# Kernel tuning notes

Measured on AMD Instinct MI355X. Metric: run time of the kernel, lower is better.

The kernel has to match this reference:

```python
import jax, jax.numpy as jnp
import numpy as np

N_NODES = 100000
N_EDGES = 1600000
IN_CH, HID_CH, OUT_CH = 128, 64, 32


def setup_inputs() -> dict:
    key = jax.random.key(0)
    k1, k2, k3, k4 = jax.random.split(key, 4)
    x = jax.random.normal(k1, (N_NODES, IN_CH), dtype=jnp.float32)
    edge_index = jax.random.randint(k2, (2, N_EDGES), 0, N_NODES, dtype=jnp.int32)
    # Glorot-ish scaling like PyG's GCNConv init
    W1 = jax.random.normal(k3, (IN_CH, HID_CH), dtype=jnp.float32) / np.sqrt(IN_CH)
    b1 = jnp.zeros((HID_CH,), dtype=jnp.float32)
    W2 = jax.random.normal(k4, (HID_CH, OUT_CH), dtype=jnp.float32) / np.sqrt(HID_CH)
    b2 = jnp.zeros((OUT_CH,), dtype=jnp.float32)
    return {"x": x, "edge_index": edge_index, "W1": W1, "b1": b1, "W2": W2, "b2": b2}


def reference(x, edge_index, W1, b1, W2, b2):
    # PyG GCNConv semantics: add self-loops, symmetric deg^{-1/2} normalization,
    # linear transform, scatter-add aggregation to destination nodes, add bias.
    N = x.shape[0]
    loops = jnp.arange(N, dtype=edge_index.dtype)
    src = jnp.concatenate([edge_index[0], loops])  # [E+N]
    dst = jnp.concatenate([edge_index[1], loops])  # [E+N]

    deg = jax.ops.segment_sum(jnp.ones_like(src, dtype=x.dtype), dst, num_segments=N)
    dis = jnp.where(deg > 0, jax.lax.rsqrt(jnp.maximum(deg, 1.0)), 0.0)  # deg^{-1/2}
    norm = (dis[src] * dis[dst])[:, None]  # [E+N, 1]

    def gcn_conv(h, W, b):
        h = h @ W                                   # [N, C_out]
        msgs = h[src] * norm                        # gather + scale, [E+N, C_out]
        return jax.ops.segment_sum(msgs, dst, num_segments=N) + b

    h = jax.nn.relu(gcn_conv(x, W1, b1))
    # dropout is identity in eval mode (training=False)
    return gcn_conv(h, W2, b2)
```

## Files before the change

### kernel.cpp

```cpp
#include <hip/hip_runtime.h>
#include <hip/hip_bf16.h>

#define IN_CH 128
#define HID_CH 64
#define OUT_CH 32
#define EPB 2048
#define MAXB 512

typedef unsigned short ushort_t;
typedef __attribute__((ext_vector_type(8))) short short8;
typedef __attribute__((ext_vector_type(4))) float float4v;

static __device__ __forceinline__ ushort_t f2bf(float f) {
    unsigned u = __float_as_uint(f);
    unsigned r = (u + 0x7fff + ((u >> 16) & 1)) >> 16;
    return (ushort_t)r;
}
static __device__ __forceinline__ float bf_lo(unsigned u) { return __uint_as_float(u << 16); }
static __device__ __forceinline__ float bf_hi(unsigned u) { return __uint_as_float(u & 0xffff0000u); }


__global__ __launch_bounds__(256) void k_partition(const int* __restrict__ src,
                                                   const int* __restrict__ dst,
                                                   int* __restrict__ gcursor,
                                                   unsigned* __restrict__ pairs,
                                                   int E, int nbk, int cap, int PB,
                                                   const float* __restrict__ W1,
                                                   unsigned* __restrict__ wsW) {
    __shared__ int lhist[MAXB];
    __shared__ int lbase[MAXB];
    __shared__ int lcur[MAXB];
    const int tid = threadIdx.x;

    if (blockIdx.x >= PB) {
        int s = (blockIdx.x - PB) * 256 + tid;
        int lane = s & 63;
        int nt = (s >> 6) & 3;
        int kc = s >> 8;
        int c = nt * 16 + (lane & 15);
        int k0 = kc * 32 + (lane >> 4) * 8;
        unsigned o[4];
#pragma unroll
        for (int d = 0; d < 4; ++d) {
            unsigned lo = f2bf(W1[(k0 + 2 * d) * 64 + c]);
            unsigned hi = f2bf(W1[(k0 + 2 * d + 1) * 64 + c]);
            o[d] = lo | (hi << 16);
        }
        ((uint4*)wsW)[s] = make_uint4(o[0], o[1], o[2], o[3]);
        return;
    }

    for (int b = tid; b < nbk; b += 256) { lhist[b] = 0; lcur[b] = 0; }
    __syncthreads();
    int s[8], d[8];
    const int e0 = blockIdx.x * EPB;
#pragma unroll
    for (int j = 0; j < 8; ++j) {
        int e = e0 + j * 256 + tid;
        if (e < E) {
            s[j] = src[e];
            d[j] = dst[e];
            atomicAdd(&lhist[d[j] >> 8], 1);
        } else {
            d[j] = -1;
        }
    }
    __syncthreads();
    for (int b = tid; b < nbk; b += 256)
        lbase[b] = lhist[b] ? atomicAdd(&gcursor[b], lhist[b]) : 0;
    __syncthreads();
#pragma unroll
    for (int j = 0; j < 8; ++j) {
        if (d[j] >= 0) {
            int b = d[j] >> 8;
            int loc = atomicAdd(&lcur[b], 1);
            int idx = lbase[b] + loc;
            if (idx < cap)
                pairs[(long long)b * cap + idx] = ((unsigned)s[j] << 8) | (unsigned)(d[j] & 255);
        }
    }
}


__global__ __launch_bounds__(256) void k_bucket_build(const unsigned* __restrict__ pairs,
                                                      const int* __restrict__ gcursor,
                                                      int* __restrict__ rowptr,
                                                      int* __restrict__ col,
                                                      float* __restrict__ dis,
                                                      int cap, int N) {
    __shared__ int lc[256];
    __shared__ int ls[256];
    __shared__ int lcur[256];
    const int b = blockIdx.x, tid = threadIdx.x;

    int ga = min(gcursor[2 * tid], cap);
    int gb = min(gcursor[2 * tid + 1], cap);
    ls[tid] = ga + gb;
    __syncthreads();
    for (int off = 1; off < 256; off <<= 1) {
        int val = (tid >= off) ? ls[tid - off] : 0;
        __syncthreads();
        ls[tid] += val;
        __syncthreads();
    }
    const int p = b >> 1;
    const int base = (p ? ls[p - 1] : 0) + ((b & 1) ? min(gcursor[b - 1], cap) : 0);
    const int total = ls[255];
    __syncthreads();
    if (b == 0 && tid == 0) rowptr[N] = total;

    lc[tid] = 0;
    __syncthreads();
    const int cnt = min(gcursor[b], cap);
    const unsigned* pp = pairs + (long long)b * cap;
    for (int i = tid; i < cnt; i += 256) atomicAdd(&lc[pp[i] & 255], 1);
    __syncthreads();
    const int v = lc[tid];
    ls[tid] = v;
    __syncthreads();
    for (int off = 1; off < 256; off <<= 1) {
        int val = (tid >= off) ? ls[tid - off] : 0;
        __syncthreads();
        ls[tid] += val;
        __syncthreads();
    }
    const int excl = ls[tid] - v;
    const int row = b * 256 + tid;
    if (row < N) {
        rowptr[row] = base + excl;
        dis[row] = rsqrtf((float)(v + 1));
    }
    lcur[tid] = base + excl;
    __syncthreads();
    for (int i = tid; i < cnt; i += 256) {
        unsigned pk = pp[i];
        int pos = atomicAdd(&lcur[pk & 255], 1);
        col[pos] = (int)(pk >> 8);
    }
}


__global__ __launch_bounds__(256) void k_mm1(const float* __restrict__ X,
                                             const unsigned* __restrict__ wsW,
                                             ushort_t* __restrict__ H, int N) {
    const int tid = threadIdx.x;
    const int wv = tid >> 6, lane = tid & 63;
    const int quad = lane >> 4, n16 = lane & 15;
    const int rowbase = blockIdx.x * 64 + wv * 16;
    const int myrow = rowbase + n16;
    const bool rok = (myrow < N);

    float4v acc0 = {}, acc1 = {}, acc2 = {}, acc3 = {};

#pragma unroll
    for (int kc = 0; kc < 4; ++kc) {
        float4 xa = make_float4(0.f, 0.f, 0.f, 0.f), xb = xa;
        if (rok) {
            const float4* p = (const float4*)(X + (long long)myrow * 128 + kc * 32 + quad * 8);
            xa = p[0];
            xb = p[1];
        }
        unsigned pk[4];
        pk[0] = (unsigned)f2bf(xa.x) | ((unsigned)f2bf(xa.y) << 16);
        pk[1] = (unsigned)f2bf(xa.z) | ((unsigned)f2bf(xa.w) << 16);
        pk[2] = (unsigned)f2bf(xb.x) | ((unsigned)f2bf(xb.y) << 16);
        pk[3] = (unsigned)f2bf(xb.z) | ((unsigned)f2bf(xb.w) << 16);
        short8 a;
        a[0] = (short)(pk[0] & 0xffff); a[1] = (short)(pk[0] >> 16);
        a[2] = (short)(pk[1] & 0xffff); a[3] = (short)(pk[1] >> 16);
        a[4] = (short)(pk[2] & 0xffff); a[5] = (short)(pk[2] >> 16);
        a[6] = (short)(pk[3] & 0xffff); a[7] = (short)(pk[3] >> 16);

        const short8* wb = (const short8*)wsW;
        short8 b0 = wb[(kc * 4 + 0) * 64 + lane];
        short8 b1 = wb[(kc * 4 + 1) * 64 + lane];
        short8 b2 = wb[(kc * 4 + 2) * 64 + lane];
        short8 b3 = wb[(kc * 4 + 3) * 64 + lane];

        acc0 = __builtin_amdgcn_mfma_f32_16x16x32_bf16(a, b0, acc0, 0, 0, 0);
        acc1 = __builtin_amdgcn_mfma_f32_16x16x32_bf16(a, b1, acc1, 0, 0, 0);
        acc2 = __builtin_amdgcn_mfma_f32_16x16x32_bf16(a, b2, acc2, 0, 0, 0);
        acc3 = __builtin_amdgcn_mfma_f32_16x16x32_bf16(a, b3, acc3, 0, 0, 0);
    }

#pragma unroll
    for (int i = 0; i < 4; ++i) {
        int row = rowbase + quad * 4 + i;
        if (row < N) {
            long long o = (long long)row * 64 + n16;
            H[o]      = f2bf(acc0[i]);
            H[o + 16] = f2bf(acc1[i]);
            H[o + 32] = f2bf(acc2[i]);
            H[o + 48] = f2bf(acc3[i]);
        }
    }
}


__global__ __launch_bounds__(256) void k_agg64_mm2(const unsigned* __restrict__ h,
                                                   const int* __restrict__ rowptr,
                                                   const int* __restrict__ col,
                                                   const float* __restrict__ dis,
                                                   const float* __restrict__ b1,
                                                   const float* __restrict__ W2,
                                                   unsigned* __restrict__ h2, int N) {
    __shared__ float zbuf[4][64];
    __shared__ float sW2[64 * 32];
    const int tid = threadIdx.x;
    for (int i = tid; i < 512; i += 256) ((float4*)sW2)[i] = ((const float4*)W2)[i];
    __syncthreads();

    const int wv = tid >> 6, lane = tid & 63;
    const int t = lane & 15, g = lane >> 4;
    const int c32 = lane & 31, kh = lane >> 5;
    const float4 bq = ((const float4*)b1)[t];

    const int wave0 = blockIdx.x * 4 + wv;
    const int nwaves = gridDim.x * 4;
    const uint2* h2w = (const uint2*)h;

    for (int row = wave0; row < N; row += nwaves) {
        const int start = rowptr[row];
        const int deg = rowptr[row + 1] - start;
        const float dr = dis[row];

        int myCol = row;
        float myDis = 0.f;
        if (lane < deg) {
            myCol = col[start + lane];
            myDis = dis[myCol];
        }

        uint2 us = h2w[row * 16 + t];
        float w0 = (g == 0) ? dr : 0.f;
        float a0 = w0 * bf_lo(us.x), a1 = w0 * bf_hi(us.x);
        float a2 = w0 * bf_lo(us.y), a3 = w0 * bf_hi(us.y);

        const int cnt = min(deg, 64);
        for (int k0 = 0; k0 < cnt; k0 += 16) {
#pragma unroll
            for (int u = 0; u < 4; ++u) {
                int slot = k0 + 4 * u + g;
                int s = __shfl(myCol, slot);
                float f = __shfl(myDis, slot);
                uint2 uu = h2w[s * 16 + t];
                a0 += f * bf_lo(uu.x); a1 += f * bf_hi(uu.x);
                a2 += f * bf_lo(uu.y); a3 += f * bf_hi(uu.y);
            }
        }
        for (int j = start + 64 + g; j < start + deg; j += 4) {
            int s = col[j];
            float f = dis[s];
            uint2 uu = h2w[s * 16 + t];
            a0 += f * bf_lo(uu.x); a1 += f * bf_hi(uu.x);
            a2 += f * bf_lo(uu.y); a3 += f * bf_hi(uu.y);
        }
        a0 += __shfl_down(a0, 32); a1 += __shfl_down(a1, 32);
        a2 += __shfl_down(a2, 32); a3 += __shfl_down(a3, 32);
        a0 += __shfl_down(a0, 16); a1 += __shfl_down(a1, 16);
        a2 += __shfl_down(a2, 16); a3 += __shfl_down(a3, 16);

        if (lane < 16) {
            float4 zq;
            zq.x = bq.x + dr * a0;
            zq.y = bq.y + dr * a1;
            zq.z = bq.z + dr * a2;
            zq.w = bq.w + dr * a3;
            *(float4*)&zbuf[wv][4 * t] = zq;
        }
        __builtin_amdgcn_wave_barrier();

        float acc = 0.f;
        const float* zp = &zbuf[wv][kh * 32];
        const float* wp = &sW2[kh * 32 * 32 + c32];
#pragma unroll
        for (int k = 0; k < 32; k += 4) {
            float4 zv = *(const float4*)(zp + k);
            acc += fmaxf(zv.x, 0.f) * wp[k * 32] + fmaxf(zv.y, 0.f) * wp[(k + 1) * 32] +
                   fmaxf(zv.z, 0.f) * wp[(k + 2) * 32] + fmaxf(zv.w, 0.f) * wp[(k + 3) * 32];
        }
        __builtin_amdgcn_wave_barrier();
        acc += __shfl_down(acc, 32);

        const int tt = lane & 15;
        float o0 = __shfl(acc, 2 * tt);
        float o1 = __shfl(acc, 2 * tt + 1);
        if (lane < 16)
            h2[row * 16 + tt] = (unsigned)f2bf(o0) | ((unsigned)f2bf(o1) << 16);
    }
}


__global__ __launch_bounds__(256) void k_agg32(const unsigned* __restrict__ h,
                                               const int* __restrict__ rowptr,
                                               const int* __restrict__ col,
                                               const float* __restrict__ dis,
                                               const float* __restrict__ b,
                                               float* __restrict__ out, int N) {
    const int wave = (blockIdx.x * 256 + threadIdx.x) >> 6;
    const int lane = threadIdx.x & 63;
    if (wave >= N) return;
    const int row = wave;
    const int t = lane & 7, g = lane >> 3;

    const int start = rowptr[row];
    const int deg = rowptr[row + 1] - start;
    const float dr = dis[row];

    int myCol = row;
    float myDis = 0.f;
    if (lane < deg) {
        myCol = col[start + lane];
        myDis = dis[myCol];
    }

    const uint2* hw = (const uint2*)h;
    uint2 us = hw[row * 8 + t];
    float w0 = (g == 0) ? dr : 0.f;
    float a0 = w0 * bf_lo(us.x), a1 = w0 * bf_hi(us.x);
    float a2 = w0 * bf_lo(us.y), a3 = w0 * bf_hi(us.y);

    const int cnt = min(deg, 64);
    for (int k0 = 0; k0 < cnt; k0 += 32) {
#pragma unroll
        for (int u = 0; u < 4; ++u) {
            int slot = k0 + 8 * u + g;
            int s = __shfl(myCol, slot);
            float f = __shfl(myDis, slot);
            uint2 uu = hw[s * 8 + t];
            a0 += f * bf_lo(uu.x); a1 += f * bf_hi(uu.x);
            a2 += f * bf_lo(uu.y); a3 += f * bf_hi(uu.y);
        }
    }
    for (int j = start + 64 + g; j < start + deg; j += 8) {
        int s = col[j];
        float f = dis[s];
        uint2 uu = hw[s * 8 + t];
        a0 += f * bf_lo(uu.x); a1 += f * bf_hi(uu.x);
        a2 += f * bf_lo(uu.y); a3 += f * bf_hi(uu.y);
    }
    a0 += __shfl_down(a0, 32); a1 += __shfl_down(a1, 32);
    a2 += __shfl_down(a2, 32); a3 += __shfl_down(a3, 32);
    a0 += __shfl_down(a0, 16); a1 += __shfl_down(a1, 16);
    a2 += __shfl_down(a2, 16); a3 += __shfl_down(a3, 16);
    a0 += __shfl_down(a0, 8);  a1 += __shfl_down(a1, 8);
    a2 += __shfl_down(a2, 8);  a3 += __shfl_down(a3, 8);

    if (lane < 8) {
        float4 bq = ((const float4*)b)[t];
        float4 o;
        o.x = bq.x + dr * a0;
        o.y = bq.y + dr * a1;
        o.z = bq.z + dr * a2;
        o.w = bq.w + dr * a3;
        ((float4*)out)[(long long)row * 8 + t] = o;
    }
}

extern "C" void kernel_launch(void* const* d_in, const int* in_sizes, int n_in,
                              void* d_out, int out_size, void* d_ws, size_t ws_size,
                              hipStream_t stream) {
    const float* x  = (const float*)d_in[0];
    const int*   ei = (const int*)d_in[1];
    const float* W1 = (const float*)d_in[2];
    const float* b1 = (const float*)d_in[3];
    const float* W2 = (const float*)d_in[4];
    const float* b2 = (const float*)d_in[5];
    float* out = (float*)d_out;

    const int N = in_sizes[0] / IN_CH;
    const int E = in_sizes[1] / 2;
    const int* esrc = ei;
    const int* edst = ei + E;

    int nbk = (N + 255) >> 8;
    if (nbk > MAXB) nbk = MAXB;
    const int per_b = (E + nbk - 1) / nbk;
    const int cap = per_b + per_b / 4 + 256;

    int* rowptr   = (int*)d_ws;
    int* gcursor  = rowptr + (((N + 1) + 15) & ~15);
    unsigned* wsW = (unsigned*)(gcursor + MAXB);
    int* col      = (int*)(wsW + 4096);
    float* dis    = (float*)(col + ((E + 15) & ~15));
    ushort_t* h1  = (ushort_t*)(dis + ((N + 15) & ~15));
    unsigned* scratch = (unsigned*)(h1 + (((long long)N * 64 + 31) & ~31LL));
    unsigned* pairs = scratch;
    unsigned* h2    = scratch;

    const int B = 256;
    const int PB = (E + EPB - 1) / EPB;

    hipMemsetAsync(gcursor, 0, MAXB * sizeof(int), stream);
    k_partition<<<PB + 4, B, 0, stream>>>(esrc, edst, gcursor, pairs, E, nbk, cap, PB, W1, wsW);
    k_bucket_build<<<nbk, B, 0, stream>>>(pairs, gcursor, rowptr, col, dis, cap, N);

    k_mm1<<<(N + 63) / 64, B, 0, stream>>>(x, wsW, h1, N);

    const int fblocks = (N + 31) / 32;
    k_agg64_mm2<<<fblocks, B, 0, stream>>>((const unsigned*)h1, rowptr, col, dis, b1, W2, h2, N);

    k_agg32<<<(int)(((long long)N * 64 + B - 1) / B), B, 0, stream>>>((const unsigned*)h2, rowptr, col, dis, b2, out, N);
}
```

Before: 249.2 us.

## Pre-scale features by source deg^-1/2 and use zero sentinel row for padding

Folds the source-side normalization factor into the producer kernels: mm1 multiplies each H row by dis[row], and agg64_mm2 scales its h2 output by dr. The aggregation kernels then do plain sums of gathered bf16 rows, with no per-neighbour dis lookup, shuffle or multiply. Padding lanes point at a zeroed sentinel row N (zeroed by earlier kernels), which lets the gather loop be unrolled to cover all 64 slots per iteration. The cost is extra rounding from scaling before the bf16 conversion, plus an added dependency of mm1 on dis. The sentinel row in h2's scratch area may overlap the pairs buffer.

```diff
diff --git a/kernel.cpp b/kernel.cpp
--- a/kernel.cpp
+++ b/kernel.cpp
@@ -87,12 +87,15 @@
                                                       int* __restrict__ rowptr,
                                                       int* __restrict__ col,
                                                       float* __restrict__ dis,
+                                                      unsigned* __restrict__ h1zero,
                                                       int cap, int N) {
     __shared__ int lc[256];
     __shared__ int ls[256];
     __shared__ int lcur[256];
     const int b = blockIdx.x, tid = threadIdx.x;
 
+    if (b == 0 && tid < 32) h1zero[tid] = 0;
+
     int ga = min(gcursor[2 * tid], cap);
     int gb = min(gcursor[2 * tid + 1], cap);
     ls[tid] = ga + gb;
@@ -142,8 +145,12 @@
 
 __global__ __launch_bounds__(256) void k_mm1(const float* __restrict__ X,
                                              const unsigned* __restrict__ wsW,
-                                             ushort_t* __restrict__ H, int N) {
+                                             const float* __restrict__ dis,
+                                             ushort_t* __restrict__ H,
+                                             unsigned* __restrict__ h2zero, int N) {
     const int tid = threadIdx.x;
+    if (blockIdx.x == 0 && tid < 16) h2zero[tid] = 0;
+
     const int wv = tid >> 6, lane = tid & 63;
     const int quad = lane >> 4, n16 = lane & 15;
     const int rowbase = blockIdx.x * 64 + wv * 16;
@@ -187,11 +194,12 @@
     for (int i = 0; i < 4; ++i) {
         int row = rowbase + quad * 4 + i;
         if (row < N) {
+            float dr = dis[row];
             long long o = (long long)row * 64 + n16;
-            H[o]      = f2bf(acc0[i]);
-            H[o + 16] = f2bf(acc1[i]);
-            H[o + 32] = f2bf(acc2[i]);
-            H[o + 48] = f2bf(acc3[i]);
+            H[o]      = f2bf(dr * acc0[i]);
+            H[o + 16] = f2bf(dr * acc1[i]);
+            H[o + 32] = f2bf(dr * acc2[i]);
+            H[o + 48] = f2bf(dr * acc3[i]);
         }
     }
 }
@@ -224,36 +232,32 @@
         const int deg = rowptr[row + 1] - start;
         const float dr = dis[row];
 
-        int myCol = row;
-        float myDis = 0.f;
-        if (lane < deg) {
-            myCol = col[start + lane];
-            myDis = dis[myCol];
-        }
+        int myCol = N;
+        if (lane < deg) myCol = col[start + lane];
 
         uint2 us = h2w[row * 16 + t];
-        float w0 = (g == 0) ? dr : 0.f;
-        float a0 = w0 * bf_lo(us.x), a1 = w0 * bf_hi(us.x);
-        float a2 = w0 * bf_lo(us.y), a3 = w0 * bf_hi(us.y);
+        float a0 = 0.f, a1 = 0.f, a2 = 0.f, a3 = 0.f;
+        if (g == 0) {
+            a0 = bf_lo(us.x); a1 = bf_hi(us.x);
+            a2 = bf_lo(us.y); a3 = bf_hi(us.y);
+        }
 
         const int cnt = min(deg, 64);
-        for (int k0 = 0; k0 < cnt; k0 += 16) {
-#pragma unroll
-            for (int u = 0; u < 4; ++u) {
+        for (int k0 = 0; k0 < cnt; k0 += 32) {
+#pragma unroll
+            for (int u = 0; u < 8; ++u) {
                 int slot = k0 + 4 * u + g;
                 int s = __shfl(myCol, slot);
-                float f = __shfl(myDis, slot);
                 uint2 uu = h2w[s * 16 + t];
-                a0 += f * bf_lo(uu.x); a1 += f * bf_hi(uu.x);
-                a2 += f * bf_lo(uu.y); a3 += f * bf_hi(uu.y);
+                a0 += bf_lo(uu.x); a1 += bf_hi(uu.x);
+                a2 += bf_lo(uu.y); a3 += bf_hi(uu.y);
             }
         }
         for (int j = start + 64 + g; j < start + deg; j += 4) {
             int s = col[j];
-            float f = dis[s];
             uint2 uu = h2w[s * 16 + t];
-            a0 += f * bf_lo(uu.x); a1 += f * bf_hi(uu.x);
-            a2 += f * bf_lo(uu.y); a3 += f * bf_hi(uu.y);
+            a0 += bf_lo(uu.x); a1 += bf_hi(uu.x);
+            a2 += bf_lo(uu.y); a3 += bf_hi(uu.y);
         }
         a0 += __shfl_down(a0, 32); a1 += __shfl_down(a1, 32);
         a2 += __shfl_down(a2, 32); a3 += __shfl_down(a3, 32);
@@ -286,7 +290,7 @@
         float o0 = __shfl(acc, 2 * tt);
         float o1 = __shfl(acc, 2 * tt + 1);
         if (lane < 16)
-            h2[row * 16 + tt] = (unsigned)f2bf(o0) | ((unsigned)f2bf(o1) << 16);
+            h2[row * 16 + tt] = (unsigned)f2bf(dr * o0) | ((unsigned)f2bf(dr * o1) << 16);
     }
 }
 
@@ -307,37 +311,33 @@
     const int deg = rowptr[row + 1] - start;
     const float dr = dis[row];
 
-    int myCol = row;
-    float myDis = 0.f;
-    if (lane < deg) {
-        myCol = col[start + lane];
-        myDis = dis[myCol];
-    }
+    int myCol = N;
+    if (lane < deg) myCol = col[start + lane];
 
     const uint2* hw = (const uint2*)h;
     uint2 us = hw[row * 8 + t];
-    float w0 = (g == 0) ? dr : 0.f;
-    float a0 = w0 * bf_lo(us.x), a1 = w0 * bf_hi(us.x);
-    float a2 = w0 * bf_lo(us.y), a3 = w0 * bf_hi(us.y);
+    float a0 = 0.f, a1 = 0.f, a2 = 0.f, a3 = 0.f;
+    if (g == 0) {
+        a0 = bf_lo(us.x); a1 = bf_hi(us.x);
+        a2 = bf_lo(us.y); a3 = bf_hi(us.y);
+    }
 
     const int cnt = min(deg, 64);
-    for (int k0 = 0; k0 < cnt; k0 += 32) {
-#pragma unroll
-        for (int u = 0; u < 4; ++u) {
+    for (int k0 = 0; k0 < cnt; k0 += 64) {
+#pragma unroll
+        for (int u = 0; u < 8; ++u) {
             int slot = k0 + 8 * u + g;
             int s = __shfl(myCol, slot);
-            float f = __shfl(myDis, slot);
             uint2 uu = hw[s * 8 + t];
-            a0 += f * bf_lo(uu.x); a1 += f * bf_hi(uu.x);
-            a2 += f * bf_lo(uu.y); a3 += f * bf_hi(uu.y);
+            a0 += bf_lo(uu.x); a1 += bf_hi(uu.x);
+            a2 += bf_lo(uu.y); a3 += bf_hi(uu.y);
         }
     }
     for (int j = start + 64 + g; j < start + deg; j += 8) {
         int s = col[j];
-        float f = dis[s];
         uint2 uu = hw[s * 8 + t];
-        a0 += f * bf_lo(uu.x); a1 += f * bf_hi(uu.x);
-        a2 += f * bf_lo(uu.y); a3 += f * bf_hi(uu.y);
+        a0 += bf_lo(uu.x); a1 += bf_hi(uu.x);
+        a2 += bf_lo(uu.y); a3 += bf_hi(uu.y);
     }
     a0 += __shfl_down(a0, 32); a1 += __shfl_down(a1, 32);
     a2 += __shfl_down(a2, 32); a3 += __shfl_down(a3, 32);
@@ -384,7 +384,7 @@
     int* col      = (int*)(wsW + 4096);
     float* dis    = (float*)(col + ((E + 15) & ~15));
     ushort_t* h1  = (ushort_t*)(dis + ((N + 15) & ~15));
-    unsigned* scratch = (unsigned*)(h1 + (((long long)N * 64 + 31) & ~31LL));
+    unsigned* scratch = (unsigned*)(h1 + (((long long)(N + 1) * 64 + 31) & ~31LL));
     unsigned* pairs = scratch;
     unsigned* h2    = scratch;
 
@@ -393,9 +393,10 @@
 
     hipMemsetAsync(gcursor, 0, MAXB * sizeof(int), stream);
     k_partition<<<PB + 4, B, 0, stream>>>(esrc, edst, gcursor, pairs, E, nbk, cap, PB, W1, wsW);
-    k_bucket_build<<<nbk, B, 0, stream>>>(pairs, gcursor, rowptr, col, dis, cap, N);
-
-    k_mm1<<<(N + 63) / 64, B, 0, stream>>>(x, wsW, h1, N);
+    k_bucket_build<<<nbk, B, 0, stream>>>(pairs, gcursor, rowptr, col, dis,
+                                          (unsigned*)(h1 + (long long)N * 64), cap, N);
+
+    k_mm1<<<(N + 63) / 64, B, 0, stream>>>(x, wsW, dis, h1, h2 + (long long)N * 16, N);
 
     const int fblocks = (N + 31) / 32;
     k_agg64_mm2<<<fblocks, B, 0, stream>>>((const unsigned*)h1, rowptr, col, dis, b1, W2, h2, N);
```

After: 247.2 us. No clear change (-0.8%).
